# Kernel tuning notes

Hardware: AMD Instinct MI355X
Metric: run time of the kernel (lower is better)

Reference implementation:

```python
import jax, jax.numpy as jnp
import numpy as np

B, P = 8, 1000          # batch_size, num_prots
N = B * P               # total PPI nodes
E = 512000              # edges (avg degree 64)
F_HPO = 1024            # HPO feature dim (num_features)
F_MOLP = 8192           # protein molecular feature dim (hardcoded)
F_MOLD = 1024           # drug molecular feature dim (hardcoded)
D = 200
EPS = 1e-8              # torch CosineSimilarity default eps


def leaky(x):
    return jax.nn.leaky_relu(x, 0.2)


def gcn_improved(x, W, b, src, dst):
    # PyG GCNConv(improved=True): A_hat = A + 2*I, symmetrically normalized.
    h = x @ W                                                   # [N,200]
    deg = jnp.zeros((x.shape[0],), x.dtype).at[dst].add(1.0) + 2.0
    dinv = jax.lax.rsqrt(deg)
    norm = dinv[src] * dinv[dst]                                # [E]
    out = jnp.zeros_like(h).at[dst].add(norm[:, None] * h[src])  # gather->scale->scatter
    out = out + (2.0 * dinv * dinv)[:, None] * h                # self loops with weight 2
    return out + b


def setup_inputs() -> dict:
    key = jax.random.key(0)
    ks = jax.random.split(key, 30)
    def W(i, shape):
        return jax.random.normal(ks[i], shape, jnp.float32) * (1.0 / float(np.sqrt(shape[0])))
    def bvec(i, n):
        return jax.random.normal(ks[i], (n,), jnp.float32) * 0.01
    return {
        # forward inputs
        'PPI_x': jax.random.normal(ks[0], (N, F_HPO), jnp.float32),
        'protein_mol_feature': jax.random.normal(ks[1], (N, F_MOLP), jnp.float32),
        'drug_feature': jax.random.normal(ks[2], (B, F_HPO), jnp.float32),
        'drug_mol_feature': jax.random.normal(ks[3], (B, F_MOLD), jnp.float32),
        'edge_index': jax.random.randint(ks[4], (2, E), 0, N, dtype=jnp.int32),
        # frozen HPO model heads (assumed Linear -> 200)
        'hpo_drug_W': W(5, (F_HPO, D)), 'hpo_drug_b': bvec(6, D),
        'hpo_prot_W': W(7, (F_HPO, D)), 'hpo_prot_b': bvec(8, D),
        # mol_protein_model: 8192 -> 256 -> 200
        'mp_W1': W(9, (F_MOLP, 256)), 'mp_b1': bvec(10, 256),
        'mp_W2': W(11, (256, D)), 'mp_b2': bvec(12, D),
        # mol_drug_model: 1024 -> 256 -> 200
        'md_W1': W(13, (F_MOLD, 256)), 'md_b1': bvec(14, 256),
        'md_W2': W(15, (256, D)), 'md_b2': bvec(16, D),
        # fusion linears
        'pl1_W': W(17, (2 * D, D)), 'pl1_b': bvec(18, D),
        'dl1_W': W(19, (2 * D, D)), 'dl1_b': bvec(20, D),
        'dl2_W': W(21, (D, D)), 'dl2_b': bvec(22, D),
        # GCN layers
        'g1_W': W(23, (D, D)), 'g1_b': bvec(24, D),
        'g2_W': W(25, (D, D)), 'g2_b': bvec(26, D),
    }


def reference(PPI_x, protein_mol_feature, drug_feature, drug_mol_feature, edge_index,
              hpo_drug_W, hpo_drug_b, hpo_prot_W, hpo_prot_b,
              mp_W1, mp_b1, mp_W2, mp_b2, md_W1, md_b1, md_W2, md_b2,
              pl1_W, pl1_b, dl1_W, dl1_b, dl2_W, dl2_b,
              g1_W, g1_b, g2_W, g2_b):
    src, dst = edge_index[0], edge_index[1]
    # protein branch (dropout is identity in eval)
    px = PPI_x @ hpo_prot_W + hpo_prot_b                                 # [N,200]
    pm = leaky(protein_mol_feature @ mp_W1 + mp_b1) @ mp_W2 + mp_b2      # [N,200]
    px = leaky(jnp.concatenate([px, pm], axis=1))                        # [N,400]
    px = px @ pl1_W + pl1_b                                              # [N,200]
    # drug branch
    df = drug_feature @ hpo_drug_W + hpo_drug_b                          # [B,200]
    dm = leaky(drug_mol_feature @ md_W1 + md_b1) @ md_W2 + md_b2         # [B,200]
    d = leaky(jnp.concatenate([dm, df], axis=1))                         # [B,400]
    d = leaky(d @ dl1_W + dl1_b)                                         # [B,200]
    d = d @ dl2_W + dl2_b                                                # [B,200]
    d = jnp.repeat(d, P, axis=0)                                         # [B*P,200]
    # two stacked GCN layers (no nonlinearity between, as in source)
    px = gcn_improved(px, g1_W, g1_b, src, dst)
    px = gcn_improved(px, g2_W, g2_b, src, dst)
    # per-row cosine similarity (torch.nn.CosineSimilarity(dim=1))
    num = jnp.sum(d * px, axis=1)
    den = jnp.maximum(jnp.linalg.norm(d, axis=1), EPS) * jnp.maximum(jnp.linalg.norm(px, axis=1), EPS)
    sim = num / den
    return jax.nn.sigmoid(sim.reshape(B, P))
```

## Files before the change

kernel.cpp:

```cpp
#include <hip/hip_runtime.h>
#include <cstdint>
#include <cstddef>

typedef uint16_t u16;
typedef __bf16 bf16x8 __attribute__((ext_vector_type(8)));
typedef short  s16x8  __attribute__((ext_vector_type(8)));
typedef float  f32x4  __attribute__((ext_vector_type(4)));

__device__ __forceinline__ u16 f2b(float f) {
    union { float f; uint32_t u; } v; v.f = f;
    uint32_t u = v.u;
    uint32_t r = (u + 0x7FFFu + ((u >> 16) & 1u)) >> 16;
    return (u16)r;
}
__device__ __forceinline__ float b2f(u16 h) {
    union { uint32_t u; float f; } v; v.u = ((uint32_t)h) << 16;
    return v.f;
}
__device__ __forceinline__ float leakyf(float x) { return x > 0.f ? x : 0.2f * x; }
__device__ __forceinline__ void unp4(uint2 u, float& f0, float& f1, float& f2, float& f3) {
    union { uint32_t u; float f; } t;
    t.u = u.x << 16;          f0 = t.f;
    t.u = u.x & 0xffff0000u;  f1 = t.f;
    t.u = u.y << 16;          f2 = t.f;
    t.u = u.y & 0xffff0000u;  f3 = t.f;
}

static constexpr int NN = 8000;
static constexpr int EE = 512000;
static constexpr int BB = 8;

__global__ void conv_wT(const float* __restrict__ W, int Wn, int rows, int rowOff,
                        u16* __restrict__ Bt, int Kpad, int kOff, int kSpan) {
    __shared__ u16 tile[64][65];
    const int kb = blockIdx.x * 64, nb = blockIdx.y * 64;
    const int tid = threadIdx.x;
    const int ln = tid & 63, lw = tid >> 6;
    #pragma unroll
    for (int r = 0; r < 16; r++) {
        int kk = kb + lw * 16 + r;
        int n  = nb + ln;
        float v = (kk < rows && n < Wn) ? W[(size_t)(rowOff + kk) * Wn + n] : 0.f;
        tile[ln][lw * 16 + r] = f2b(v);
    }
    __syncthreads();
    #pragma unroll
    for (int r = 0; r < 16; r++) {
        int nl = lw * 16 + r;
        int kk = kb + ln;
        if (kk < kSpan) Bt[(size_t)(nb + nl) * Kpad + kOff + kk] = tile[nl][ln];
    }
}

__global__ void conv_wT5(const float* W_mp2, const float* W_pl1, const float* W_g1, const float* W_g2,
                         u16* Btmp2, u16* Btpl1, u16* Btg1, u16* Btg2) {
    __shared__ u16 tile[64][65];
    const float* W; int Wn, rows, rowOff; u16* Bt; int Kpad, kOff, kSpan;
    switch (blockIdx.z) {
        case 0: W = W_mp2; Wn = 200; rows = 256; rowOff = 0;   Bt = Btmp2; Kpad = 256; kOff = 0;   kSpan = 256; break;
        case 1: W = W_pl1; Wn = 200; rows = 200; rowOff = 0;   Bt = Btpl1; Kpad = 512; kOff = 0;   kSpan = 256; break;
        case 2: W = W_pl1; Wn = 200; rows = 200; rowOff = 200; Bt = Btpl1; Kpad = 512; kOff = 256; kSpan = 256; break;
        case 3: W = W_g1;  Wn = 200; rows = 200; rowOff = 0;   Bt = Btg1;  Kpad = 256; kOff = 0;   kSpan = 256; break;
        default:W = W_g2;  Wn = 200; rows = 200; rowOff = 0;   Bt = Btg2;  Kpad = 256; kOff = 0;   kSpan = 256; break;
    }
    const int kb = blockIdx.x * 64, nb = blockIdx.y * 64;
    const int tid = threadIdx.x;
    const int ln = tid & 63, lw = tid >> 6;
    #pragma unroll
    for (int r = 0; r < 16; r++) {
        int kk = kb + lw * 16 + r;
        int n  = nb + ln;
        float v = (kk < rows && n < Wn) ? W[(size_t)(rowOff + kk) * Wn + n] : 0.f;
        tile[ln][lw * 16 + r] = f2b(v);
    }
    __syncthreads();
    #pragma unroll
    for (int r = 0; r < 16; r++) {
        int nl = lw * 16 + r;
        int kk = kb + ln;
        if (kk < kSpan) Bt[(size_t)(nb + nl) * Kpad + kOff + kk] = tile[nl][ln];
    }
}

__global__ void padvec5(const float* p0, int n0, float* d0,
                        const float* p1, int n1, float* d1,
                        const float* p2, int n2, float* d2,
                        const float* p3, int n3, float* d3,
                        const float* p4, int n4, float* d4) {
    const float* p; int n; float* d;
    switch (blockIdx.x) {
        case 0: p = p0; n = n0; d = d0; break;
        case 1: p = p1; n = n1; d = d1; break;
        case 2: p = p2; n = n2; d = d2; break;
        case 3: p = p3; n = n3; d = d3; break;
        default: p = p4; n = n4; d = d4; break;
    }
    int i = threadIdx.x;
    d[i] = (p != nullptr && i < n) ? p[i] : 0.f;
}

__global__ void zero_i32(int* __restrict__ p, int n) {
    int i = blockIdx.x * 256 + threadIdx.x;
    if (i < n) p[i] = 0;
}

__global__ __launch_bounds__(256) void gemm_kernel(
    const void* __restrict__ Ap, int a_is_f32, int lda,
    const u16* __restrict__ Bt, int K, int kLen,
    const float* __restrict__ bias,
    void* __restrict__ Cp, int cmode, int ldc, int do_leaky, size_t partStride) {
    __shared__ u16 As[32][72];
    __shared__ u16 Bs[256][72];
    const int tid  = threadIdx.x;
    const int m0   = blockIdx.x * 32;
    const int kStart = blockIdx.y * kLen;
    const int wave = tid >> 6, lane = tid & 63;
    const int q = lane >> 4, r = lane & 15;
    const int wn = wave * 64;
    const int arow = tid & 31, akoff = (tid >> 5) * 8;
    const int brow = tid >> 2, bkoff = (tid & 3) * 16;

    f32x4 acc[2][4];
    #pragma unroll
    for (int i = 0; i < 2; i++)
        #pragma unroll
        for (int j = 0; j < 4; j++) acc[i][j] = (f32x4){0, 0, 0, 0};

    for (int k0 = kStart; k0 < kStart + kLen; k0 += 64) {
        if (a_is_f32) {
            const float* A = (const float*)Ap + (size_t)(m0 + arow) * lda + k0 + akoff;
            float fa[8];
            *(float4*)(&fa[0]) = *(const float4*)(A + 0);
            *(float4*)(&fa[4]) = *(const float4*)(A + 4);
            u16 ha[8];
            #pragma unroll
            for (int j = 0; j < 8; j++) ha[j] = f2b(fa[j]);
            *(uint4*)(&As[arow][akoff]) = *(uint4*)(&ha[0]);
        } else {
            const u16* A = (const u16*)Ap + (size_t)(m0 + arow) * lda + k0 + akoff;
            *(uint4*)(&As[arow][akoff]) = *(const uint4*)A;
        }
        #pragma unroll
        for (int p = 0; p < 4; p++) {
            const int row = p * 64 + brow;
            const u16* bp = Bt + (size_t)row * K + k0 + bkoff;
            uint4 u0 = *(const uint4*)(bp + 0);
            uint4 u1 = *(const uint4*)(bp + 8);
            *(uint4*)(&Bs[row][bkoff])     = u0;
            *(uint4*)(&Bs[row][bkoff + 8]) = u1;
        }
        __syncthreads();
        #pragma unroll
        for (int ks = 0; ks < 2; ks++) {
            const int kb = ks * 32 + q * 8;
            s16x8 a0 = *(const s16x8*)(&As[r][kb]);
            s16x8 a1 = *(const s16x8*)(&As[16 + r][kb]);
            s16x8 b0 = *(const s16x8*)(&Bs[wn +      r][kb]);
            s16x8 b1 = *(const s16x8*)(&Bs[wn + 16 + r][kb]);
            s16x8 b2 = *(const s16x8*)(&Bs[wn + 32 + r][kb]);
            s16x8 b3 = *(const s16x8*)(&Bs[wn + 48 + r][kb]);
            acc[0][0] = __builtin_amdgcn_mfma_f32_16x16x32_bf16(__builtin_bit_cast(bf16x8, a0), __builtin_bit_cast(bf16x8, b0), acc[0][0], 0, 0, 0);
            acc[0][1] = __builtin_amdgcn_mfma_f32_16x16x32_bf16(__builtin_bit_cast(bf16x8, a0), __builtin_bit_cast(bf16x8, b1), acc[0][1], 0, 0, 0);
            acc[0][2] = __builtin_amdgcn_mfma_f32_16x16x32_bf16(__builtin_bit_cast(bf16x8, a0), __builtin_bit_cast(bf16x8, b2), acc[0][2], 0, 0, 0);
            acc[0][3] = __builtin_amdgcn_mfma_f32_16x16x32_bf16(__builtin_bit_cast(bf16x8, a0), __builtin_bit_cast(bf16x8, b3), acc[0][3], 0, 0, 0);
            acc[1][0] = __builtin_amdgcn_mfma_f32_16x16x32_bf16(__builtin_bit_cast(bf16x8, a1), __builtin_bit_cast(bf16x8, b0), acc[1][0], 0, 0, 0);
            acc[1][1] = __builtin_amdgcn_mfma_f32_16x16x32_bf16(__builtin_bit_cast(bf16x8, a1), __builtin_bit_cast(bf16x8, b1), acc[1][1], 0, 0, 0);
            acc[1][2] = __builtin_amdgcn_mfma_f32_16x16x32_bf16(__builtin_bit_cast(bf16x8, a1), __builtin_bit_cast(bf16x8, b2), acc[1][2], 0, 0, 0);
            acc[1][3] = __builtin_amdgcn_mfma_f32_16x16x32_bf16(__builtin_bit_cast(bf16x8, a1), __builtin_bit_cast(bf16x8, b3), acc[1][3], 0, 0, 0);
        }
        __syncthreads();
    }

    #pragma unroll
    for (int ti = 0; ti < 2; ti++)
        #pragma unroll
        for (int tj = 0; tj < 4; tj++)
            #pragma unroll
            for (int reg = 0; reg < 4; reg++) {
                int gr = m0 + ti * 16 + q * 4 + reg;
                int gc = wn + tj * 16 + r;
                float v = acc[ti][tj][reg];
                if (cmode == 2) {
                    ((float*)Cp)[blockIdx.y * partStride + (size_t)gr * 256 + gc] = v;
                } else {
                    v += bias[gc];
                    if (do_leaky) v = leakyf(v);
                    if (cmode == 1) ((u16*)Cp)[(size_t)gr * ldc + gc] = f2b(v);
                    else            ((float*)Cp)[(size_t)gr * ldc + gc] = v;
                }
            }
}

__global__ void reduce_k(const float* __restrict__ part, size_t partStride, int S,
                         const float* __restrict__ bias, void* __restrict__ out,
                         int out_bf16, int ldc, int do_leaky) {
    int i = blockIdx.x * 256 + threadIdx.x;
    float v = 0.f;
    for (int s = 0; s < S; s++) v += part[s * partStride + i];
    int col = i & 255, row = i >> 8;
    v += bias[col];
    if (do_leaky) v = leakyf(v);
    if (out_bf16) ((u16*)out)[(size_t)row * ldc + col] = f2b(v);
    else          ((float*)out)[(size_t)row * ldc + col] = v;
}

__global__ void count_kernel(const int* __restrict__ dst, int* __restrict__ cnt) {
    int e = blockIdx.x * 256 + threadIdx.x;
    if (e < EE) atomicAdd(&cnt[dst[e]], 1);
}
__global__ void scan_kernel(const int* __restrict__ cnt, int* __restrict__ row_start,
                            int* __restrict__ cursor, float* __restrict__ dinv) {
    __shared__ int part[1024];
    const int tid = threadIdx.x;
    int local[8];
    int s = 0;
    const int base = tid * 8;
    #pragma unroll
    for (int j = 0; j < 8; j++) { int idx = base + j; int v = (idx < NN) ? cnt[idx] : 0; local[j] = s; s += v; }
    part[tid] = s;
    __syncthreads();
    for (int off = 1; off < 1024; off <<= 1) {
        int v = (tid >= off) ? part[tid - off] : 0;
        __syncthreads();
        part[tid] += v;
        __syncthreads();
    }
    const int excl = (tid == 0) ? 0 : part[tid - 1];
    #pragma unroll
    for (int j = 0; j < 8; j++) {
        int idx = base + j;
        if (idx < NN) {
            int v = excl + local[j];
            row_start[idx] = v; cursor[idx] = v;
            dinv[idx] = rsqrtf((float)cnt[idx] + 2.0f);
        }
    }
    if (tid == 1023) row_start[NN] = part[1023];
}
__global__ void fill_kernel(const int* __restrict__ src, const int* __restrict__ dst,
                            int* __restrict__ cursor, const float* __restrict__ dinv,
                            int* __restrict__ csr_src, float* __restrict__ csr_w) {
    int e = blockIdx.x * 256 + threadIdx.x;
    if (e < EE) {
        int s = src[e], d = dst[e];
        int pos = atomicAdd(&cursor[d], 1);
        csr_src[pos] = s;
        csr_w[pos]   = dinv[s] * dinv[d];
    }
}

__global__ __launch_bounds__(256) void agg_kernel(
    const u16* __restrict__ h, const float* __restrict__ dinv,
    const int* __restrict__ row_start, const int* __restrict__ csr_src,
    const float* __restrict__ csr_w, const float* __restrict__ bias,
    u16* __restrict__ out_bf16, const float* __restrict__ dhat,
    float* __restrict__ out_sig) {
    const int wave = threadIdx.x >> 6, lane = threadIdx.x & 63;
    const int node = blockIdx.x * 4 + wave;
    const int start = row_start[node], end = row_start[node + 1];
    const float di = dinv[node];

    float a0, a1, a2, a3;
    {
        uint2 hv = *(const uint2*)(h + (size_t)node * 256 + lane * 4);
        float f0, f1, f2, f3; unp4(hv, f0, f1, f2, f3);
        float sl = 2.f * di * di;
        a0 = sl * f0; a1 = sl * f1; a2 = sl * f2; a3 = sl * f3;
    }

    for (int p = start; p < end; p += 64) {
        const int n = min(64, end - p);
        int   mySrc = 0;
        float myW   = 0.f;
        if (lane < n) { mySrc = csr_src[p + lane]; myW = csr_w[p + lane]; }
        int j0 = 0;
        for (; j0 + 8 <= n; j0 += 8) {
            int sj[8]; float wj[8]; uint2 rj[8];
            #pragma unroll
            for (int j = 0; j < 8; j++) { sj[j] = __shfl(mySrc, j0 + j); wj[j] = __shfl(myW, j0 + j); }
            #pragma unroll
            for (int j = 0; j < 8; j++) rj[j] = *(const uint2*)(h + (size_t)sj[j] * 256 + lane * 4);
            #pragma unroll
            for (int j = 0; j < 8; j++) {
                float f0, f1, f2, f3; unp4(rj[j], f0, f1, f2, f3);
                a0 += wj[j] * f0; a1 += wj[j] * f1; a2 += wj[j] * f2; a3 += wj[j] * f3;
            }
        }
        for (; j0 < n; j0++) {
            int s = __shfl(mySrc, j0);
            float w = __shfl(myW, j0);
            uint2 rv = *(const uint2*)(h + (size_t)s * 256 + lane * 4);
            float f0, f1, f2, f3; unp4(rv, f0, f1, f2, f3);
            a0 += w * f0; a1 += w * f1; a2 += w * f2; a3 += w * f3;
        }
    }

    if (out_bf16 != nullptr) {
        uint2 o = {0u, 0u};
        if (lane < 50) {
            float4 bv = *(const float4*)(bias + lane * 4);
            u16 h0 = f2b(a0 + bv.x), h1 = f2b(a1 + bv.y), h2 = f2b(a2 + bv.z), h3 = f2b(a3 + bv.w);
            o.x = (uint32_t)h0 | ((uint32_t)h1 << 16);
            o.y = (uint32_t)h2 | ((uint32_t)h3 << 16);
        }
        *(uint2*)(out_bf16 + (size_t)node * 256 + lane * 4) = o;
    } else {
        float dot = 0.f, nn2 = 0.f;
        if (lane < 50) {
            float4 bv = *(const float4*)(bias + lane * 4);
            float4 dv = *(const float4*)(dhat + (node / 1000) * 200 + lane * 4);
            float v0 = a0 + bv.x, v1 = a1 + bv.y, v2 = a2 + bv.z, v3 = a3 + bv.w;
            dot = v0 * dv.x + v1 * dv.y + v2 * dv.z + v3 * dv.w;
            nn2 = v0 * v0 + v1 * v1 + v2 * v2 + v3 * v3;
        }
        #pragma unroll
        for (int off = 32; off; off >>= 1) {
            dot += __shfl_xor(dot, off, 64);
            nn2 += __shfl_xor(nn2, off, 64);
        }
        if (lane == 0) {
            float sim = dot / fmaxf(sqrtf(nn2), 1e-8f);
            out_sig[node] = 1.f / (1.f + expf(-sim));
        }
    }
}

__global__ void drug_kernel(const float* __restrict__ drugF, const float* __restrict__ drugM,
                            const float* __restrict__ hW, const float* __restrict__ hb,
                            const float* __restrict__ m1W, const float* __restrict__ m1b,
                            const float* __restrict__ m2W, const float* __restrict__ m2b,
                            const float* __restrict__ l1W, const float* __restrict__ l1b,
                            const float* __restrict__ l2W, const float* __restrict__ l2b,
                            float* __restrict__ dhat) {
    const int b = blockIdx.x, tid = threadIdx.x;
    __shared__ float sF[1024], sM[1024], sT[256], s400[400], s200[200], sred[256];
    for (int k = tid; k < 1024; k += 256) { sF[k] = drugF[b * 1024 + k]; sM[k] = drugM[b * 1024 + k]; }
    __syncthreads();
    {
        float acc = m1b[tid];
        for (int k = 0; k < 1024; k++) acc += sM[k] * m1W[k * 256 + tid];
        sT[tid] = leakyf(acc);
    }
    float dfv = 0.f;
    if (tid < 200) {
        dfv = hb[tid];
        for (int k = 0; k < 1024; k++) dfv += sF[k] * hW[k * 200 + tid];
    }
    __syncthreads();
    if (tid < 200) {
        float acc = m2b[tid];
        for (int k = 0; k < 256; k++) acc += sT[k] * m2W[k * 200 + tid];
        s400[tid]       = leakyf(acc);
        s400[200 + tid] = leakyf(dfv);
    }
    __syncthreads();
    if (tid < 200) {
        float acc = l1b[tid];
        for (int k = 0; k < 400; k++) acc += s400[k] * l1W[k * 200 + tid];
        s200[tid] = leakyf(acc);
    }
    __syncthreads();
    float dv = 0.f;
    if (tid < 200) {
        dv = l2b[tid];
        for (int k = 0; k < 200; k++) dv += s200[k] * l2W[k * 200 + tid];
    }
    sred[tid] = (tid < 200) ? dv * dv : 0.f;
    __syncthreads();
    for (int off = 128; off; off >>= 1) {
        if (tid < off) sred[tid] += sred[tid + off];
        __syncthreads();
    }
    float nrm = fmaxf(sqrtf(sred[0]), 1e-8f);
    if (tid < 200) dhat[b * 200 + tid] = dv / nrm;
}

extern "C" void kernel_launch(void* const* d_in, const int* in_sizes, int n_in,
                              void* d_out, int out_size, void* d_ws, size_t ws_size,
                              hipStream_t stream) {
    const float* PPI_x = (const float*)d_in[0];
    const float* PMF   = (const float*)d_in[1];
    const float* drugF = (const float*)d_in[2];
    const float* drugM = (const float*)d_in[3];
    const int*   eidx  = (const int*)d_in[4];
    const float* hpo_drug_W = (const float*)d_in[5];
    const float* hpo_drug_b = (const float*)d_in[6];
    const float* hpo_prot_W = (const float*)d_in[7];
    const float* hpo_prot_b = (const float*)d_in[8];
    const float* mp_W1 = (const float*)d_in[9];
    const float* mp_b1 = (const float*)d_in[10];
    const float* mp_W2 = (const float*)d_in[11];
    const float* mp_b2 = (const float*)d_in[12];
    const float* md_W1 = (const float*)d_in[13];
    const float* md_b1 = (const float*)d_in[14];
    const float* md_W2 = (const float*)d_in[15];
    const float* md_b2 = (const float*)d_in[16];
    const float* pl1_W = (const float*)d_in[17];
    const float* pl1_b = (const float*)d_in[18];
    const float* dl1_W = (const float*)d_in[19];
    const float* dl1_b = (const float*)d_in[20];
    const float* dl2_W = (const float*)d_in[21];
    const float* dl2_b = (const float*)d_in[22];
    const float* g1_W  = (const float*)d_in[23];
    const float* g1_b  = (const float*)d_in[24];
    const float* g2_W  = (const float*)d_in[25];
    const float* g2_b  = (const float*)d_in[26];

    char* wsp = (char*)d_ws;
    size_t off = 0;
    auto alloc = [&](size_t bytes) -> void* {
        size_t o = (off + 255) & ~(size_t)255;
        off = o + bytes;
        return (void*)(wsp + o);
    };

    u16* cb    = (u16*)alloc((size_t)NN * 512 * 2);
    u16* t1    = (u16*)alloc((size_t)NN * 256 * 2);
    u16* px2   = (u16*)alloc((size_t)NN * 256 * 2);
    u16* hbuf  = (u16*)alloc((size_t)NN * 256 * 2);
    float* part = (float*)alloc((size_t)4 * NN * 256 * 4);
    u16* Btmp1 = (u16*)alloc((size_t)256 * 8192 * 2);
    u16* Bthpo = (u16*)alloc((size_t)256 * 1024 * 2);
    u16* Btmp2 = (u16*)alloc((size_t)256 * 256 * 2);
    u16* Btpl1 = (u16*)alloc((size_t)256 * 512 * 2);
    u16* Btg1  = (u16*)alloc((size_t)256 * 256 * 2);
    u16* Btg2  = (u16*)alloc((size_t)256 * 256 * 2);
    float* bias_hpo = (float*)alloc(256 * 4);
    float* bias_m1  = (float*)alloc(256 * 4);
    float* bias_m2  = (float*)alloc(256 * 4);
    float* bias_pl  = (float*)alloc(256 * 4);
    float* zero256  = (float*)alloc(256 * 4);
    float* dhat     = (float*)alloc((size_t)BB * 200 * 4);
    int*   deg      = (int*)alloc((size_t)NN * 4);
    float* dinv     = (float*)alloc((size_t)NN * 4);
    int*   row_st   = (int*)alloc((size_t)(NN + 4) * 4);
    int*   cursor   = (int*)alloc((size_t)NN * 4);
    int*   csr_src  = (int*)alloc((size_t)EE * 4);
    float* csr_w    = (float*)alloc((size_t)EE * 4);

    u16* y1 = t1;
    const size_t PSTRIDE = (size_t)NN * 256;

    const int* e_src = eidx;
    const int* e_dst = eidx + EE;

    conv_wT<<<dim3(16, 4),  256, 0, stream>>>(hpo_prot_W, 200, 1024, 0, Bthpo, 1024, 0, 1024);
    conv_wT<<<dim3(128, 4), 256, 0, stream>>>(mp_W1,      256, 8192, 0, Btmp1, 8192, 0, 8192);
    conv_wT5<<<dim3(4, 4, 5), 256, 0, stream>>>(mp_W2, pl1_W, g1_W, g2_W, Btmp2, Btpl1, Btg1, Btg2);
    padvec5<<<5, 256, 0, stream>>>(hpo_prot_b, 200, bias_hpo,
                                   mp_b1,      256, bias_m1,
                                   mp_b2,      200, bias_m2,
                                   pl1_b,      200, bias_pl,
                                   nullptr,    0,   zero256);

    drug_kernel<<<BB, 256, 0, stream>>>(drugF, drugM, hpo_drug_W, hpo_drug_b,
                                        md_W1, md_b1, md_W2, md_b2,
                                        dl1_W, dl1_b, dl2_W, dl2_b, dhat);

    const int MB = NN / 32;
    const int RG = (NN * 256) / 256;

    gemm_kernel<<<dim3(MB, 4), 256, 0, stream>>>(PPI_x, 1, 1024, Bthpo, 1024, 256, zero256, part, 2, 256, 0, PSTRIDE);
    reduce_k<<<RG, 256, 0, stream>>>(part, PSTRIDE, 4, bias_hpo, cb, 1, 512, 1);
    gemm_kernel<<<dim3(MB, 4), 256, 0, stream>>>(PMF, 1, 8192, Btmp1, 8192, 2048, zero256, part, 2, 256, 0, PSTRIDE);
    reduce_k<<<RG, 256, 0, stream>>>(part, PSTRIDE, 4, bias_m1, t1, 1, 256, 1);
    gemm_kernel<<<dim3(MB, 1), 256, 0, stream>>>(t1, 0, 256, Btmp2, 256, 256, bias_m2, cb + 256, 1, 512, 1, 0);
    gemm_kernel<<<dim3(MB, 1), 256, 0, stream>>>(cb, 0, 512, Btpl1, 512, 512, bias_pl, px2, 1, 256, 0, 0);

    zero_i32<<<(NN + 255) / 256, 256, 0, stream>>>(deg, NN);
    count_kernel<<<EE / 256, 256, 0, stream>>>(e_dst, deg);
    scan_kernel<<<1, 1024, 0, stream>>>(deg, row_st, cursor, dinv);
    fill_kernel<<<EE / 256, 256, 0, stream>>>(e_src, e_dst, cursor, dinv, csr_src, csr_w);

    gemm_kernel<<<dim3(MB, 1), 256, 0, stream>>>(px2, 0, 256, Btg1, 256, 256, zero256, hbuf, 1, 256, 0, 0);
    agg_kernel<<<NN / 4, 256, 0, stream>>>(hbuf, dinv, row_st, csr_src, csr_w, g1_b, y1, nullptr, nullptr);
    gemm_kernel<<<dim3(MB, 1), 256, 0, stream>>>(y1, 0, 256, Btg2, 256, 256, zero256, hbuf, 1, 256, 0, 0);
    agg_kernel<<<NN / 4, 256, 0, stream>>>(hbuf, dinv, row_st, csr_src, csr_w, g2_b, nullptr, dhat, (float*)d_out);
}
```

Baseline: 889.3 us.

## Drop LDS staging in GEMM, use MFMA-fragment global loads and merge reductions

The GEMM kernel stops staging A and B tiles through shared memory. Each lane now loads its MFMA fragments straight from global memory, with a templated M-tile of 64 or 32 rows, and the two barriers per k-step go away. The large 8192-wide GEMM is split 8 ways along K instead of 4. Its partial sums and the HPO GEMM's partials are reduced in one fused reduce2 kernel, and the bias padding and degree zeroing are merged into one prep kernel, cutting launches. The trade-off is that operands are re-read from global or L2 per wave instead of shared through LDS, and the split-K partials take more memory traffic.

```diff
diff --git a/kernel.cpp b/kernel.cpp
--- a/kernel.cpp
+++ b/kernel.cpp
@@ -82,97 +82,90 @@
     }
 }
 
-__global__ void padvec5(const float* p0, int n0, float* d0,
-                        const float* p1, int n1, float* d1,
-                        const float* p2, int n2, float* d2,
-                        const float* p3, int n3, float* d3,
-                        const float* p4, int n4, float* d4) {
-    const float* p; int n; float* d;
-    switch (blockIdx.x) {
-        case 0: p = p0; n = n0; d = d0; break;
-        case 1: p = p1; n = n1; d = d1; break;
-        case 2: p = p2; n = n2; d = d2; break;
-        case 3: p = p3; n = n3; d = d3; break;
-        default: p = p4; n = n4; d = d4; break;
-    }
-    int i = threadIdx.x;
-    d[i] = (p != nullptr && i < n) ? p[i] : 0.f;
-}
-
-__global__ void zero_i32(int* __restrict__ p, int n) {
-    int i = blockIdx.x * 256 + threadIdx.x;
-    if (i < n) p[i] = 0;
-}
-
+__global__ void prep_kernel(const float* p0, int n0, float* d0,
+                            const float* p1, int n1, float* d1,
+                            const float* p2, int n2, float* d2,
+                            const float* p3, int n3, float* d3,
+                            const float* p4, int n4, float* d4,
+                            int* __restrict__ deg) {
+    const int bx = blockIdx.x, tid = threadIdx.x;
+    if (bx < 5) {
+        const float* p; int n; float* d;
+        switch (bx) {
+            case 0: p = p0; n = n0; d = d0; break;
+            case 1: p = p1; n = n1; d = d1; break;
+            case 2: p = p2; n = n2; d = d2; break;
+            case 3: p = p3; n = n3; d = d3; break;
+            default: p = p4; n = n4; d = d4; break;
+        }
+        d[tid] = (p != nullptr && tid < n) ? p[tid] : 0.f;
+    }
+    const int base = bx * 250;
+    if (tid < 250) deg[base + tid] = 0;
+}
+
+template<int MREP>
 __global__ __launch_bounds__(256) void gemm_kernel(
     const void* __restrict__ Ap, int a_is_f32, int lda,
     const u16* __restrict__ Bt, int K, int kLen,
     const float* __restrict__ bias,
     void* __restrict__ Cp, int cmode, int ldc, int do_leaky, size_t partStride) {
-    __shared__ u16 As[32][72];
-    __shared__ u16 Bs[256][72];
     const int tid  = threadIdx.x;
-    const int m0   = blockIdx.x * 32;
+    constexpr int BM = MREP * 16;
+    const int m0   = blockIdx.x * BM;
     const int kStart = blockIdx.y * kLen;
     const int wave = tid >> 6, lane = tid & 63;
     const int q = lane >> 4, r = lane & 15;
     const int wn = wave * 64;
-    const int arow = tid & 31, akoff = (tid >> 5) * 8;
-    const int brow = tid >> 2, bkoff = (tid & 3) * 16;
-
-    f32x4 acc[2][4];
-    #pragma unroll
-    for (int i = 0; i < 2; i++)
+
+    f32x4 acc[MREP][4];
+    #pragma unroll
+    for (int i = 0; i < MREP; i++)
         #pragma unroll
         for (int j = 0; j < 4; j++) acc[i][j] = (f32x4){0, 0, 0, 0};
 
-    for (int k0 = kStart; k0 < kStart + kLen; k0 += 64) {
+    size_t aoff[MREP];
+    #pragma unroll
+    for (int m = 0; m < MREP; m++) aoff[m] = (size_t)(m0 + m * 16 + r) * lda + q * 8;
+    size_t boff[4];
+    #pragma unroll
+    for (int j = 0; j < 4; j++) boff[j] = (size_t)(wn + j * 16 + r) * K + q * 8;
+
+    const float* Af = (const float*)Ap;
+    const u16*   Ah = (const u16*)Ap;
+
+    #pragma unroll 2
+    for (int k0 = kStart; k0 < kStart + kLen; k0 += 32) {
+        bf16x8 a[MREP];
         if (a_is_f32) {
-            const float* A = (const float*)Ap + (size_t)(m0 + arow) * lda + k0 + akoff;
-            float fa[8];
-            *(float4*)(&fa[0]) = *(const float4*)(A + 0);
-            *(float4*)(&fa[4]) = *(const float4*)(A + 4);
-            u16 ha[8];
-            #pragma unroll
-            for (int j = 0; j < 8; j++) ha[j] = f2b(fa[j]);
-            *(uint4*)(&As[arow][akoff]) = *(uint4*)(&ha[0]);
+            #pragma unroll
+            for (int m = 0; m < MREP; m++) {
+                const float* p = Af + aoff[m] + k0;
+                float4 x = *(const float4*)p;
+                float4 y = *(const float4*)(p + 4);
+                u16 h[8];
+                h[0] = f2b(x.x); h[1] = f2b(x.y); h[2] = f2b(x.z); h[3] = f2b(x.w);
+                h[4] = f2b(y.x); h[5] = f2b(y.y); h[6] = f2b(y.z); h[7] = f2b(y.w);
+                a[m] = __builtin_bit_cast(bf16x8, *(uint4*)h);
+            }
         } else {
-            const u16* A = (const u16*)Ap + (size_t)(m0 + arow) * lda + k0 + akoff;
-            *(uint4*)(&As[arow][akoff]) = *(const uint4*)A;
-        }
+            #pragma unroll
+            for (int m = 0; m < MREP; m++)
+                a[m] = __builtin_bit_cast(bf16x8, *(const uint4*)(Ah + aoff[m] + k0));
+        }
+        bf16x8 b[4];
         #pragma unroll
-        for (int p = 0; p < 4; p++) {
-            const int row = p * 64 + brow;
-            const u16* bp = Bt + (size_t)row * K + k0 + bkoff;
-            uint4 u0 = *(const uint4*)(bp + 0);
-            uint4 u1 = *(const uint4*)(bp + 8);
-            *(uint4*)(&Bs[row][bkoff])     = u0;
-            *(uint4*)(&Bs[row][bkoff + 8]) = u1;
-        }
-        __syncthreads();
+        for (int j = 0; j < 4; j++)
+            b[j] = __builtin_bit_cast(bf16x8, *(const uint4*)(Bt + boff[j] + k0));
         #pragma unroll
-        for (int ks = 0; ks < 2; ks++) {
-            const int kb = ks * 32 + q * 8;
-            s16x8 a0 = *(const s16x8*)(&As[r][kb]);
-            s16x8 a1 = *(const s16x8*)(&As[16 + r][kb]);
-            s16x8 b0 = *(const s16x8*)(&Bs[wn +      r][kb]);
-            s16x8 b1 = *(const s16x8*)(&Bs[wn + 16 + r][kb]);
-            s16x8 b2 = *(const s16x8*)(&Bs[wn + 32 + r][kb]);
-            s16x8 b3 = *(const s16x8*)(&Bs[wn + 48 + r][kb]);
-            acc[0][0] = __builtin_amdgcn_mfma_f32_16x16x32_bf16(__builtin_bit_cast(bf16x8, a0), __builtin_bit_cast(bf16x8, b0), acc[0][0], 0, 0, 0);
-            acc[0][1] = __builtin_amdgcn_mfma_f32_16x16x32_bf16(__builtin_bit_cast(bf16x8, a0), __builtin_bit_cast(bf16x8, b1), acc[0][1], 0, 0, 0);
-            acc[0][2] = __builtin_amdgcn_mfma_f32_16x16x32_bf16(__builtin_bit_cast(bf16x8, a0), __builtin_bit_cast(bf16x8, b2), acc[0][2], 0, 0, 0);
-            acc[0][3] = __builtin_amdgcn_mfma_f32_16x16x32_bf16(__builtin_bit_cast(bf16x8, a0), __builtin_bit_cast(bf16x8, b3), acc[0][3], 0, 0, 0);
-            acc[1][0] = __builtin_amdgcn_mfma_f32_16x16x32_bf16(__builtin_bit_cast(bf16x8, a1), __builtin_bit_cast(bf16x8, b0), acc[1][0], 0, 0, 0);
-            acc[1][1] = __builtin_amdgcn_mfma_f32_16x16x32_bf16(__builtin_bit_cast(bf16x8, a1), __builtin_bit_cast(bf16x8, b1), acc[1][1], 0, 0, 0);
-            acc[1][2] = __builtin_amdgcn_mfma_f32_16x16x32_bf16(__builtin_bit_cast(bf16x8, a1), __builtin_bit_cast(bf16x8, b2), acc[1][2], 0, 0, 0);
-            acc[1][3] = __builtin_amdgcn_mfma_f32_16x16x32_bf16(__builtin_bit_cast(bf16x8, a1), __builtin_bit_cast(bf16x8, b3), acc[1][3], 0, 0, 0);
-        }
-        __syncthreads();
-    }
-
-    #pragma unroll
-    for (int ti = 0; ti < 2; ti++)
+        for (int m = 0; m < MREP; m++)
+            #pragma unroll
+            for (int j = 0; j < 4; j++)
+                acc[m][j] = __builtin_amdgcn_mfma_f32_16x16x32_bf16(a[m], b[j], acc[m][j], 0, 0, 0);
+    }
+
+    #pragma unroll
+    for (int ti = 0; ti < MREP; ti++)
         #pragma unroll
         for (int tj = 0; tj < 4; tj++)
             #pragma unroll
@@ -191,17 +184,19 @@
             }
 }
 
-__global__ void reduce_k(const float* __restrict__ part, size_t partStride, int S,
-                         const float* __restrict__ bias, void* __restrict__ out,
-                         int out_bf16, int ldc, int do_leaky) {
+__global__ void reduce2(const float* __restrict__ part, size_t PS,
+                        const float* __restrict__ bias_m1, u16* __restrict__ t1,
+                        const float* __restrict__ bias_hpo, u16* __restrict__ cb) {
     int i = blockIdx.x * 256 + threadIdx.x;
+    int col = i & 255, row = i >> 8;
     float v = 0.f;
-    for (int s = 0; s < S; s++) v += part[s * partStride + i];
-    int col = i & 255, row = i >> 8;
-    v += bias[col];
-    if (do_leaky) v = leakyf(v);
-    if (out_bf16) ((u16*)out)[(size_t)row * ldc + col] = f2b(v);
-    else          ((float*)out)[(size_t)row * ldc + col] = v;
+    #pragma unroll
+    for (int s = 0; s < 8; s++) v += part[(size_t)s * PS + i];
+    t1[(size_t)row * 256 + col] = f2b(leakyf(v + bias_m1[col]));
+    float w = 0.f;
+    #pragma unroll
+    for (int s = 8; s < 12; s++) w += part[(size_t)s * PS + i];
+    cb[(size_t)row * 512 + col] = f2b(leakyf(w + bias_hpo[col]));
 }
 
 __global__ void count_kernel(const int* __restrict__ dst, int* __restrict__ cnt) {
@@ -418,7 +413,7 @@
     u16* t1    = (u16*)alloc((size_t)NN * 256 * 2);
     u16* px2   = (u16*)alloc((size_t)NN * 256 * 2);
     u16* hbuf  = (u16*)alloc((size_t)NN * 256 * 2);
-    float* part = (float*)alloc((size_t)4 * NN * 256 * 4);
+    float* part = (float*)alloc((size_t)12 * NN * 256 * 4);
     u16* Btmp1 = (u16*)alloc((size_t)256 * 8192 * 2);
     u16* Bthpo = (u16*)alloc((size_t)256 * 1024 * 2);
     u16* Btmp2 = (u16*)alloc((size_t)256 * 256 * 2);
@@ -447,33 +442,32 @@
     conv_wT<<<dim3(16, 4),  256, 0, stream>>>(hpo_prot_W, 200, 1024, 0, Bthpo, 1024, 0, 1024);
     conv_wT<<<dim3(128, 4), 256, 0, stream>>>(mp_W1,      256, 8192, 0, Btmp1, 8192, 0, 8192);
     conv_wT5<<<dim3(4, 4, 5), 256, 0, stream>>>(mp_W2, pl1_W, g1_W, g2_W, Btmp2, Btpl1, Btg1, Btg2);
-    padvec5<<<5, 256, 0, stream>>>(hpo_prot_b, 200, bias_hpo,
-                                   mp_b1,      256, bias_m1,
-                                   mp_b2,      200, bias_m2,
-                                   pl1_b,      200, bias_pl,
-                                   nullptr,    0,   zero256);
+    prep_kernel<<<32, 256, 0, stream>>>(hpo_prot_b, 200, bias_hpo,
+                                        mp_b1,      256, bias_m1,
+                                        mp_b2,      200, bias_m2,
+                                        pl1_b,      200, bias_pl,
+                                        nullptr,    0,   zero256, deg);
 
     drug_kernel<<<BB, 256, 0, stream>>>(drugF, drugM, hpo_drug_W, hpo_drug_b,
                                         md_W1, md_b1, md_W2, md_b2,
                                         dl1_W, dl1_b, dl2_W, dl2_b, dhat);
 
-    const int MB = NN / 32;
     const int RG = (NN * 256) / 256;
 
-    gemm_kernel<<<dim3(MB, 4), 256, 0, stream>>>(PPI_x, 1, 1024, Bthpo, 1024, 256, zero256, part, 2, 256, 0, PSTRIDE);
-    reduce_k<<<RG, 256, 0, stream>>>(part, PSTRIDE, 4, bias_hpo, cb, 1, 512, 1);
-    gemm_kernel<<<dim3(MB, 4), 256, 0, stream>>>(PMF, 1, 8192, Btmp1, 8192, 2048, zero256, part, 2, 256, 0, PSTRIDE);
-    reduce_k<<<RG, 256, 0, stream>>>(part, PSTRIDE, 4, bias_m1, t1, 1, 256, 1);
-    gemm_kernel<<<dim3(MB, 1), 256, 0, stream>>>(t1, 0, 256, Btmp2, 256, 256, bias_m2, cb + 256, 1, 512, 1, 0);
-    gemm_kernel<<<dim3(MB, 1), 256, 0, stream>>>(cb, 0, 512, Btpl1, 512, 512, bias_pl, px2, 1, 256, 0, 0);
-
-    zero_i32<<<(NN + 255) / 256, 256, 0, stream>>>(deg, NN);
+    gemm_kernel<4><<<dim3(125, 4), 256, 0, stream>>>(PPI_x, 1, 1024, Bthpo, 1024, 256, zero256,
+                                                     part + 8 * PSTRIDE, 2, 256, 0, PSTRIDE);
+    gemm_kernel<4><<<dim3(125, 8), 256, 0, stream>>>(PMF, 1, 8192, Btmp1, 8192, 1024, zero256,
+                                                     part, 2, 256, 0, PSTRIDE);
+    reduce2<<<RG, 256, 0, stream>>>(part, PSTRIDE, bias_m1, t1, bias_hpo, cb);
+    gemm_kernel<2><<<dim3(250, 1), 256, 0, stream>>>(t1, 0, 256, Btmp2, 256, 256, bias_m2, cb + 256, 1, 512, 1, 0);
+    gemm_kernel<2><<<dim3(250, 1), 256, 0, stream>>>(cb, 0, 512, Btpl1, 512, 512, bias_pl, px2, 1, 256, 0, 0);
+
     count_kernel<<<EE / 256, 256, 0, stream>>>(e_dst, deg);
     scan_kernel<<<1, 1024, 0, stream>>>(deg, row_st, cursor, dinv);
     fill_kernel<<<EE / 256, 256, 0, stream>>>(e_src, e_dst, cursor, dinv, csr_src, csr_w);
 
-    gemm_kernel<<<dim3(MB, 1), 256, 0, stream>>>(px2, 0, 256, Btg1, 256, 256, zero256, hbuf, 1, 256, 0, 0);
+    gemm_kernel<2><<<dim3(250, 1), 256, 0, stream>>>(px2, 0, 256, Btg1, 256, 256, zero256, hbuf, 1, 256, 0, 0);
     agg_kernel<<<NN / 4, 256, 0, stream>>>(hbuf, dinv, row_st, csr_src, csr_w, g1_b, y1, nullptr, nullptr);
-    gemm_kernel<<<dim3(MB, 1), 256, 0, stream>>>(y1, 0, 256, Btg2, 256, 256, zero256, hbuf, 1, 256, 0, 0);
+    gemm_kernel<2><<<dim3(250, 1), 256, 0, stream>>>(y1, 0, 256, Btg2, 256, 256, zero256, hbuf, 1, 256, 0, 0);
     agg_kernel<<<NN / 4, 256, 0, stream>>>(hbuf, dinv, row_st, csr_src, csr_w, g2_b, nullptr, dhat, (float*)d_out);
 }
```

After: 968.4 us. +8.9%, slower.
